# Optimization experiments

Measured on AMD Instinct MI355X. Metric: run time of the kernel, lower is better.

The kernel has to match this reference:

```python
import jax, jax.numpy as jnp
import numpy as np

C = 768
NH = 8
S_SP = 9            # spatial size per axis; seq = 9**3 = 729
HID = (C * 4 * 2) // 3  # 2048, floor(768*8/3)
E = 3               # num_experts
TOPK = 2
EPS = 1e-5


def setup_inputs() -> dict:
    key = jax.random.key(0)
    ks = jax.random.split(key, 10)
    b = 8
    p = lambda k, shape: (jax.random.normal(k, shape, dtype=jnp.float32) * 0.02)
    return {
        "x": jax.random.normal(ks[0], (b, C, S_SP, S_SP, S_SP), dtype=jnp.float32),
        "ln_w": jnp.ones((C, S_SP, S_SP, S_SP), dtype=jnp.float32),
        "ln_b": jnp.zeros((C, S_SP, S_SP, S_SP), dtype=jnp.float32),
        "qkv_w": p(ks[1], (C, 3 * C)),
        "proj_w": p(ks[2], (C, C)),
        "router_w": p(ks[3], (C, E)),
        "gate_w": p(ks[4], (E, C, HID)),
        "up_w": p(ks[5], (E, C, HID)),
        "down_w": p(ks[6], (E, HID, C)),
    }


def _ablock(x, ln_w, ln_b, qkv_w, proj_w, router_w, gate_w, up_w, down_w):
    b, c, t, h, w = x.shape
    s = t * h * w
    dh = c // NH

    # LayerNorm over normalized_shape = (c, t, h, w)
    mean = jnp.mean(x, axis=(1, 2, 3, 4), keepdims=True)
    var = jnp.var(x, axis=(1, 2, 3, 4), keepdims=True)
    y = (x - mean) * jax.lax.rsqrt(var + EPS) * ln_w + ln_b

    # Attention (note: source applies NO 1/sqrt(dh) scaling)
    tok = jnp.transpose(y.reshape(b, c, s), (0, 2, 1))        # (b, s, c)
    qkv = (tok @ qkv_w).reshape(b, s, 3, NH, dh)
    qkv = jnp.transpose(qkv, (2, 0, 3, 1, 4))                  # (3, b, nh, s, dh)
    q, k, v = qkv[0], qkv[1], qkv[2]
    attn = jax.nn.softmax(jnp.einsum("bhsd,bhtd->bhst", q, k), axis=-1)
    o = jnp.einsum("bhst,bhtd->bhsd", attn, v)
    o = jnp.transpose(o, (0, 2, 1, 3)).reshape(b, s, c) @ proj_w  # (b, s, c)
    x = x + jnp.transpose(o, (0, 2, 1)).reshape(b, c, t, h, w)

    # MoE with top-2 routing over SwiGLU experts (dense compute)
    tok = jnp.transpose(x.reshape(b, c, s), (0, 2, 1))         # (b, s, c)
    probs = jax.nn.softmax(tok @ router_w, axis=-1)            # (b, s, E)
    vals, idx = jax.lax.top_k(probs, TOPK)
    vals = vals / jnp.sum(vals, axis=-1, keepdims=True)
    wfull = jnp.sum(jax.nn.one_hot(idx, E, dtype=tok.dtype) * vals[..., None], axis=2)  # (b, s, E)

    g = jnp.einsum("bsc,ech->bseh", tok, gate_w)
    u = jnp.einsum("bsc,ech->bseh", tok, up_w)
    hid = jax.nn.silu(g) * u                                   # (b, s, E, HID)
    eo = jnp.einsum("bseh,ehc->bsec", hid, down_w)             # (b, s, E, c)
    moe_out = jnp.einsum("bsec,bse->bsc", eo, wfull)

    return x + jnp.transpose(moe_out, (0, 2, 1)).reshape(b, c, t, h, w)


def reference(x, ln_w, ln_b, qkv_w, proj_w, router_w, gate_w, up_w, down_w):
    return _ablock(x, ln_w, ln_b, qkv_w, proj_w, router_w, gate_w, up_w, down_w)
```

## Files before the change

kernel.cpp:

```cpp
#include <hip/hip_runtime.h>
#include <hip/hip_bf16.h>

#define C_    768
#define NH_   8
#define DH_   96
#define S_    729
#define B_    8
#define MTOK  5832
#define C3    2304
#define GUN   12288
#define DK    6144
#define SPAD  736
#define NPB   559872

typedef __attribute__((ext_vector_type(8))) short short8;
typedef __attribute__((ext_vector_type(4))) float f32x4;
typedef __attribute__((ext_vector_type(4))) unsigned int uint4v;
typedef __hip_bfloat16 bf16;

__device__ __forceinline__ void gld_lds16(const bf16* g, bf16* l) {
  __builtin_amdgcn_global_load_lds((const __attribute__((address_space(1))) void*)g,
                                   (__attribute__((address_space(3))) void*)l, 16, 0, 0);
}
__device__ __forceinline__ void gld_lds16c(const char* g, char* l) {
  __builtin_amdgcn_global_load_lds((const __attribute__((address_space(1))) void*)g,
                                   (__attribute__((address_space(3))) void*)l, 16, 0, 0);
}

template<int DB>
__device__ __forceinline__ void tile_step(
    char* ldsc, char* ldsw,
    const int rA0, const int rA1, const int rB0, const int rB1,
    const char* pA0, const char* pA1, const char* pA2, const char* pA3,
    const char* pB0, const char* pB1, const char* pB2, const char* pB3,
    const int s1, const int s2, const bool gH1, const bool gH0, const int wmode,
    f32x4 (&acc)[8][4], short8 (&a4)[4][2], short8 (&b4)[4][2])
{
  const int DBO = DB * 65536;
  const int NBO = 65536 - DBO;
  #pragma unroll
  for (int mf = 0; mf < 4; ++mf) {
    a4[mf][0] = *(const short8*)(ldsc + DBO + rA0 + mf*2048);
    a4[mf][1] = *(const short8*)(ldsc + DBO + rA1 + mf*2048);
  }
  #pragma unroll
  for (int nf = 0; nf < 4; ++nf) {
    b4[nf][0] = *(const short8*)(ldsc + DBO + rB0 + nf*2048);
    b4[nf][1] = *(const short8*)(ldsc + DBO + rB1 + nf*2048);
  }
  if (gH1) {
    gld_lds16c(pA2 + s1, ldsw + NBO + 16384);
    gld_lds16c(pA3 + s1, ldsw + NBO + 16384 + 8192);
    gld_lds16c(pB2 + s1, ldsw + NBO + 32768 + 16384);
    gld_lds16c(pB3 + s1, ldsw + NBO + 32768 + 16384 + 8192);
  }
  __builtin_amdgcn_s_setprio(1);
  #pragma unroll
  for (int mf = 0; mf < 4; ++mf)
    #pragma unroll
    for (int nf = 0; nf < 4; ++nf)
      #pragma unroll
      for (int j = 0; j < 2; ++j)
        acc[mf][nf] = __builtin_amdgcn_mfma_f32_16x16x32_bf16(a4[mf][j], b4[nf][j], acc[mf][nf], 0, 0, 0);
  __builtin_amdgcn_s_setprio(0);
  __builtin_amdgcn_s_barrier();
  #pragma unroll
  for (int mi = 0; mi < 4; ++mi) {
    a4[mi][0] = *(const short8*)(ldsc + DBO + rA0 + (4+mi)*2048);
    a4[mi][1] = *(const short8*)(ldsc + DBO + rA1 + (4+mi)*2048);
  }
  __builtin_amdgcn_s_barrier();
  if (gH0) {
    gld_lds16c(pB0 + s2, ldsw + DBO + 32768);
    gld_lds16c(pB1 + s2, ldsw + DBO + 32768 + 8192);
    gld_lds16c(pA0 + s2, ldsw + DBO);
    gld_lds16c(pA1 + s2, ldsw + DBO + 8192);
  }
  __builtin_amdgcn_s_setprio(1);
  #pragma unroll
  for (int mi = 0; mi < 4; ++mi)
    #pragma unroll
    for (int nf = 0; nf < 4; ++nf)
      #pragma unroll
      for (int j = 0; j < 2; ++j)
        acc[4+mi][nf] = __builtin_amdgcn_mfma_f32_16x16x32_bf16(a4[mi][j], b4[nf][j], acc[4+mi][nf], 0, 0, 0);
  __builtin_amdgcn_s_setprio(0);
  if (wmode == 0)      asm volatile("s_waitcnt vmcnt(4)" ::: "memory");
  else if (wmode == 1) asm volatile("s_waitcnt vmcnt(0)" ::: "memory");
  __builtin_amdgcn_s_barrier();
}

__global__ void __launch_bounds__(512, 2)
gemm8(const bf16* __restrict__ A, long a_rs,
      const bf16* __restrict__ Bt, long b_rs,
      float* __restrict__ Cf, bf16* __restrict__ Cb,
      long c_rs, long c_zoff, int M, int N, int Ksub,
      const float* __restrict__ wfull, int mode)
{
  __shared__ __attribute__((aligned(128))) char ldsc[131072];
  const int tid = threadIdx.x;
  const int wid = tid >> 6, lid = tid & 63;
  const int wm = wid >> 2, wn = wid & 3;
  const int fr = lid & 15, g8 = (lid >> 4) * 8;
  const int brow = blockIdx.y * 256, bcol = blockIdx.x * 256;
  const long k0b = (long)blockIdx.z * Ksub * 2;
  const long a_rsb = a_rs * 2, b_rsb = b_rs * 2;
  const int srow = tid >> 3;
  const int scol = ((tid & 7) ^ (srow & 7)) << 4;
  const int NT = Ksub >> 6;
  char* ldsw = ldsc + wid * 1024;

  int ra0_ = brow + srow;        if (ra0_ > M-1) ra0_ = M-1;
  int ra1_ = brow + 64 + srow;   if (ra1_ > M-1) ra1_ = M-1;
  int ra2_ = brow + 128 + srow;  if (ra2_ > M-1) ra2_ = M-1;
  int ra3_ = brow + 192 + srow;  if (ra3_ > M-1) ra3_ = M-1;
  int rb0_ = bcol + srow;        if (rb0_ > N-1) rb0_ = N-1;
  int rb1_ = bcol + 64 + srow;   if (rb1_ > N-1) rb1_ = N-1;
  int rb2_ = bcol + 128 + srow;  if (rb2_ > N-1) rb2_ = N-1;
  int rb3_ = bcol + 192 + srow;  if (rb3_ > N-1) rb3_ = N-1;
  const char* pA0 = (const char*)A + (long)ra0_*a_rsb + k0b + scol;
  const char* pA1 = (const char*)A + (long)ra1_*a_rsb + k0b + scol;
  const char* pA2 = (const char*)A + (long)ra2_*a_rsb + k0b + scol;
  const char* pA3 = (const char*)A + (long)ra3_*a_rsb + k0b + scol;
  const char* pB0 = (const char*)Bt + (long)rb0_*b_rsb + k0b + scol;
  const char* pB1 = (const char*)Bt + (long)rb1_*b_rsb + k0b + scol;
  const char* pB2 = (const char*)Bt + (long)rb2_*b_rsb + k0b + scol;
  const char* pB3 = (const char*)Bt + (long)rb3_*b_rsb + k0b + scol;

  const int swz = (fr & 7) << 4;
  const int cx0 = (g8 * 2) ^ swz;
  const int cx1 = (64 + g8 * 2) ^ swz;
  const int rA0 = (wm*128 + fr)*128 + cx0;
  const int rA1 = (wm*128 + fr)*128 + cx1;
  const int rB0 = 32768 + (wn*64 + fr)*128 + cx0;
  const int rB1 = 32768 + (wn*64 + fr)*128 + cx1;

  f32x4 acc[8][4] = {};
  short8 a4[4][2], b4[4][2];

  gld_lds16c(pA0, ldsw);
  gld_lds16c(pA1, ldsw + 8192);
  gld_lds16c(pA2, ldsw + 16384);
  gld_lds16c(pA3, ldsw + 16384 + 8192);
  gld_lds16c(pB0, ldsw + 32768);
  gld_lds16c(pB1, ldsw + 32768 + 8192);
  gld_lds16c(pB2, ldsw + 32768 + 16384);
  gld_lds16c(pB3, ldsw + 32768 + 16384 + 8192);
  gld_lds16c(pA0 + 128, ldsw + 65536);
  gld_lds16c(pA1 + 128, ldsw + 65536 + 8192);
  gld_lds16c(pB0 + 128, ldsw + 65536 + 32768);
  gld_lds16c(pB1 + 128, ldsw + 65536 + 32768 + 8192);
  asm volatile("s_waitcnt vmcnt(4)" ::: "memory");
  __builtin_amdgcn_s_barrier();

  for (int tp = 0; tp < NT; tp += 2) {
    const bool g2 = (tp + 2) < NT;
    tile_step<0>(ldsc, ldsw, rA0, rA1, rB0, rB1,
                 pA0, pA1, pA2, pA3, pB0, pB1, pB2, pB3,
                 128, 256, true, g2, g2 ? 0 : 1, acc, a4, b4);
    tile_step<1>(ldsc, ldsw, rA0, rA1, rB0, rB1,
                 pA0, pA1, pA2, pA3, pB0, pB1, pB2, pB3,
                 256, 384, g2, g2, g2 ? 0 : 2, acc, a4, b4);
    if (g2) {
      pA0 += 256; pA1 += 256; pA2 += 256; pA3 += 256;
      pB0 += 256; pB1 += 256; pB2 += 256; pB3 += 256;
    }
  }

  const int rg = (lid >> 4) * 4;
  if (mode == 3) {
    #pragma unroll
    for (int mf = 0; mf < 8; ++mf) {
      #pragma unroll
      for (int np = 0; np < 2; ++np) {
        const int hb = (bcol + wn*64 + np*32) >> 5;
        const int h = hb*16 + fr;
        const int e = h >> 11;
        #pragma unroll
        for (int j = 0; j < 4; ++j) {
          const int row = brow + wm*128 + mf*16 + rg + j;
          if (row < M) {
            float g = acc[mf][2*np][j];
            float u = acc[mf][2*np+1][j];
            float w = wfull[row*3 + e];
            float sg = g / (1.f + __expf(-g));
            Cb[(long)row*c_rs + h] = __float2bfloat16(sg * u * w);
          }
        }
      }
    }
  } else {
    #pragma unroll
    for (int mf = 0; mf < 8; ++mf) {
      #pragma unroll
      for (int nf = 0; nf < 4; ++nf) {
        const int col = bcol + wn*64 + nf*16 + fr;
        if (col < N) {
          #pragma unroll
          for (int j = 0; j < 4; ++j) {
            const int row = brow + wm*128 + mf*16 + rg + j;
            if (row < M) {
              long off = (long)blockIdx.z*c_zoff + (long)row*c_rs + col;
              if (mode == 0) Cb[off] = __float2bfloat16(acc[mf][nf][j]);
              else           Cf[off] = acc[mf][nf][j];
            }
          }
        }
      }
    }
  }
}

__global__ void __launch_bounds__(256)
gemm3_bt(const bf16* __restrict__ Ah, const bf16* __restrict__ Al,
         long a_rs, long a_oo, long a_oi,
         const bf16* __restrict__ Bth, const bf16* __restrict__ Btl,
         long b_rs, long b_oo, long b_oi,
         float* __restrict__ Cf, bf16* __restrict__ Ch, bf16* __restrict__ Cl,
         long c_rs, long c_oo, long c_oi,
         int M, int N, int K, int nlim, int zdiv)
{
  __shared__ bf16 lAh[4096];
  __shared__ bf16 lAl[4096];
  __shared__ bf16 lBh[4096];
  __shared__ bf16 lBl[4096];
  const int tid = threadIdx.x;
  const int wid = tid >> 6;
  const int lid = tid & 63;
  const int z = blockIdx.z;
  const int zo = z / zdiv, zi = z - zo*zdiv;
  const long aoff = (long)zo*a_oo + (long)zi*a_oi;
  const long boff = (long)zo*b_oo + (long)zi*b_oi;
  const long cbase = (long)zo*c_oo + (long)zi*c_oi;
  const int brow = blockIdx.y * 128;
  const int bcol = blockIdx.x * 128;

  const int ch0 = tid, ch1 = tid + 256;
  int ra0 = brow + (ch0 >> 2); if (ra0 > M-1) ra0 = M-1;
  int ra1 = brow + (ch1 >> 2); if (ra1 > M-1) ra1 = M-1;
  int rb0 = bcol + (ch0 >> 2); if (rb0 > N-1) rb0 = N-1;
  int rb1 = bcol + (ch1 >> 2); if (rb1 > N-1) rb1 = N-1;
  const int sw = ((ch0 ^ (ch0 >> 2)) & 3) * 8;
  const long ia0 = aoff + (long)ra0*a_rs + sw;
  const long ia1 = aoff + (long)ra1*a_rs + sw;
  const long ib0 = boff + (long)rb0*b_rs + sw;
  const long ib1 = boff + (long)rb1*b_rs + sw;
  bf16* dAh0 = (bf16*)((char*)lAh + wid*1024);
  bf16* dAh1 = (bf16*)((char*)lAh + 4096 + wid*1024);
  bf16* dAl0 = (bf16*)((char*)lAl + wid*1024);
  bf16* dAl1 = (bf16*)((char*)lAl + 4096 + wid*1024);
  bf16* dBh0 = (bf16*)((char*)lBh + wid*1024);
  bf16* dBh1 = (bf16*)((char*)lBh + 4096 + wid*1024);
  bf16* dBl0 = (bf16*)((char*)lBl + wid*1024);
  bf16* dBl1 = (bf16*)((char*)lBl + 4096 + wid*1024);

  f32x4 acc[4][4] = {};
  const int wm = wid >> 1, wn = wid & 1;
  const int fr = lid & 15, g8 = (lid >> 4) * 8;
  const int gx = g8 ^ ((lid & 3) << 3);

  for (int kt = 0; kt < K; kt += 32) {
    __syncthreads();
    gld_lds16(Ah + ia0 + kt, dAh0);
    gld_lds16(Ah + ia1 + kt, dAh1);
    gld_lds16(Al + ia0 + kt, dAl0);
    gld_lds16(Al + ia1 + kt, dAl1);
    gld_lds16(Bth + ib0 + kt, dBh0);
    gld_lds16(Bth + ib1 + kt, dBh1);
    gld_lds16(Btl + ib0 + kt, dBl0);
    gld_lds16(Btl + ib1 + kt, dBl1);
    __syncthreads();
    short8 fah[4], fal[4], fbh[4], fbl[4];
    #pragma unroll
    for (int m = 0; m < 4; ++m) {
      int ro = (wm*64 + m*16 + fr)*32 + gx;
      fah[m] = *(const short8*)&lAh[ro];
      fal[m] = *(const short8*)&lAl[ro];
    }
    #pragma unroll
    for (int n = 0; n < 4; ++n) {
      int ro = (wn*64 + n*16 + fr)*32 + gx;
      fbh[n] = *(const short8*)&lBh[ro];
      fbl[n] = *(const short8*)&lBl[ro];
    }
    #pragma unroll
    for (int m = 0; m < 4; ++m)
      #pragma unroll
      for (int n = 0; n < 4; ++n) {
        acc[m][n] = __builtin_amdgcn_mfma_f32_16x16x32_bf16(fal[m], fbh[n], acc[m][n], 0, 0, 0);
        acc[m][n] = __builtin_amdgcn_mfma_f32_16x16x32_bf16(fah[m], fbl[n], acc[m][n], 0, 0, 0);
        acc[m][n] = __builtin_amdgcn_mfma_f32_16x16x32_bf16(fah[m], fbh[n], acc[m][n], 0, 0, 0);
      }
  }

  const int rg = (lid >> 4) * 4;
  #pragma unroll
  for (int m = 0; m < 4; ++m) {
    #pragma unroll
    for (int n = 0; n < 4; ++n) {
      const int col = bcol + wn*64 + n*16 + fr;
      if (col < nlim) {
        #pragma unroll
        for (int j = 0; j < 4; ++j) {
          const int row = brow + wm*64 + m*16 + rg + j;
          if (row < M) {
            long off = cbase + (long)row*c_rs + col;
            float v = acc[m][n][j];
            if (Cl) {
              bf16 h = __float2bfloat16(v);
              Ch[off] = h;
              Cl[off] = __float2bfloat16(v - __bfloat162float(h));
            } else if (Ch) {
              Ch[off] = __float2bfloat16(v);
            } else {
              Cf[off] = v;
            }
          }
        }
      }
    }
  }
}

__global__ void wtrans(const float* __restrict__ in, bf16* __restrict__ out,
                       int R, int Cc, long in_rs, long out_rs, long in_bs, long out_bs,
                       int ilv, int radd)
{
  __shared__ float tile[32][33];
  in  += (long)blockIdx.z * in_bs;
  out += (long)blockIdx.z * out_bs;
  int r0 = blockIdx.y*32, c0 = blockIdx.x*32;
  int tx = threadIdx.x, ty = threadIdx.y;
  #pragma unroll
  for (int i = 0; i < 32; i += 8) {
    int r = r0 + ty + i, c = c0 + tx;
    if (r < R && c < Cc) tile[ty+i][tx] = in[(long)r*in_rs + c];
  }
  __syncthreads();
  #pragma unroll
  for (int i = 0; i < 32; i += 8) {
    int ro = c0 + ty + i, co = r0 + tx;
    if (ro < Cc && co < R) {
      int rr = ilv ? (((ro >> 4) << 5) + (ro & 15) + radd) : ro;
      out[(long)rr*out_rs + co] = __float2bfloat16(tile[tx][ty+i]);
    }
  }
}

__global__ void wtrans3(const float* __restrict__ in, bf16* __restrict__ oh, bf16* __restrict__ ol,
                        int R, int Cc, long in_rs, long out_rs)
{
  __shared__ float tile[32][33];
  int r0 = blockIdx.y*32, c0 = blockIdx.x*32;
  int tx = threadIdx.x, ty = threadIdx.y;
  #pragma unroll
  for (int i = 0; i < 32; i += 8) {
    int r = r0 + ty + i, c = c0 + tx;
    if (r < R && c < Cc) tile[ty+i][tx] = in[(long)r*in_rs + c];
  }
  __syncthreads();
  #pragma unroll
  for (int i = 0; i < 32; i += 8) {
    int ro = c0 + ty + i, co = r0 + tx;
    if (ro < Cc && co < R) {
      float v = tile[tx][ty+i];
      bf16 h = __float2bfloat16(v);
      long o = (long)ro*out_rs + co;
      oh[o] = h;
      ol[o] = __float2bfloat16(v - __bfloat162float(h));
    }
  }
}

__global__ void ln_partial(const float* __restrict__ x, float* __restrict__ part) {
  int b = blockIdx.y, blk = blockIdx.x;
  const float* xb = x + (long)b*NPB;
  int start = blk * 4374;
  float s = 0.f, ss = 0.f;
  for (int i = start + threadIdx.x; i < start + 4374; i += 256) {
    float v = xb[i]; s += v; ss += v*v;
  }
  #pragma unroll
  for (int o = 32; o; o >>= 1) { s += __shfl_down(s, o); ss += __shfl_down(ss, o); }
  __shared__ float red[2][4];
  int wid = threadIdx.x >> 6, lid = threadIdx.x & 63;
  if (lid == 0) { red[0][wid] = s; red[1][wid] = ss; }
  __syncthreads();
  if (threadIdx.x == 0) {
    float S = 0.f, SS = 0.f;
    for (int w = 0; w < 4; ++w) { S += red[0][w]; SS += red[1][w]; }
    part[(b*128 + blk)*2] = S; part[(b*128 + blk)*2 + 1] = SS;
  }
}

__global__ void ln_final(const float* __restrict__ part, float* __restrict__ stats) {
  int b = blockIdx.x, lid = threadIdx.x;
  float s = 0.f, ss = 0.f;
  for (int i = lid; i < 128; i += 64) { s += part[(b*128+i)*2]; ss += part[(b*128+i)*2+1]; }
  #pragma unroll
  for (int o = 32; o; o >>= 1) { s += __shfl_down(s, o); ss += __shfl_down(ss, o); }
  if (lid == 0) {
    float mean = s / (float)NPB;
    float var = ss / (float)NPB - mean*mean;
    stats[b*2] = mean; stats[b*2+1] = rsqrtf(var + 1e-5f);
  }
}

__global__ void ln_apply3(const float* __restrict__ x, const float* __restrict__ lnw,
                          const float* __restrict__ lnb, const float* __restrict__ stats,
                          bf16* __restrict__ th, bf16* __restrict__ tl, long ts)
{
  __shared__ float tile[32][33];
  int b = blockIdx.z;
  int s0 = blockIdx.x*32, c0 = blockIdx.y*32;
  float mean = stats[b*2], rstd = stats[b*2+1];
  int tx = threadIdx.x, ty = threadIdx.y;
  #pragma unroll
  for (int i = 0; i < 32; i += 8) {
    int c = c0 + ty + i, s = s0 + tx;
    if (s < S_) {
      long o = (long)c*S_ + s;
      tile[ty+i][tx] = (x[(long)b*NPB + o] - mean)*rstd*lnw[o] + lnb[o];
    }
  }
  __syncthreads();
  #pragma unroll
  for (int i = 0; i < 32; i += 8) {
    int s = s0 + ty + i, c = c0 + tx;
    if (s < S_) {
      float v = tile[tx][ty+i];
      bf16 h = __float2bfloat16(v);
      long o = ((long)b*S_ + s)*ts + c;
      th[o] = h;
      tl[o] = __float2bfloat16(v - __bfloat162float(h));
    }
  }
}

__global__ void vtrans2(const bf16* __restrict__ qkvh, const bf16* __restrict__ qkvl,
                        bf16* __restrict__ VTh, bf16* __restrict__ VTl)
{
  __shared__ float tile[32][33];
  int z = blockIdx.z;
  const bf16* qkv = (z < 64) ? qkvh : qkvl;
  bf16* VT = (z < 64) ? VTh : VTl;
  int zz = z & 63;
  int bb = zz >> 3, h = zz & 7;
  const bf16* v = qkv + (long)bb*S_*C3 + 1536 + h*DH_;
  bf16* o = VT + (long)zz*DH_*SPAD;
  int t0 = blockIdx.y*32, d0 = blockIdx.x*32;
  int tx = threadIdx.x, ty = threadIdx.y;
  #pragma unroll
  for (int i = 0; i < 32; i += 8) {
    int t = t0 + ty + i, d = d0 + tx;
    float val = 0.f;
    if (t < S_ && d < DH_) val = __bfloat162float(v[(long)t*C3 + d]);
    tile[ty+i][tx] = val;
  }
  __syncthreads();
  #pragma unroll
  for (int i = 0; i < 32; i += 8) {
    int d = d0 + ty + i, t = t0 + tx;
    if (d < DH_ && t < SPAD) o[(long)d*SPAD + t] = __float2bfloat16(tile[tx][ty+i]);
  }
}

__global__ void softmax3p(bf16* __restrict__ scores, int nrows) {
  int row = blockIdx.x*4 + (threadIdx.x >> 6);
  if (row >= nrows) return;
  int lid = threadIdx.x & 63;
  bf16* ph = scores + (long)row*2*SPAD;
  bf16* pl = ph + SPAD;
  float vals[12];
  float mx = -1e30f;
  #pragma unroll
  for (int i = 0; i < 12; ++i) {
    int t = i*64 + lid;
    float v = -1e30f;
    if (t < S_) v = __bfloat162float(ph[t]) + __bfloat162float(pl[t]);
    vals[i] = v; mx = fmaxf(mx, v);
  }
  #pragma unroll
  for (int o = 32; o; o >>= 1) mx = fmaxf(mx, __shfl_xor(mx, o));
  float sum = 0.f;
  #pragma unroll
  for (int i = 0; i < 12; ++i) { float e = __expf(vals[i] - mx); vals[i] = e; sum += e; }
  #pragma unroll
  for (int o = 32; o; o >>= 1) sum += __shfl_xor(sum, o);
  float inv = 1.f / sum;
  #pragma unroll
  for (int i = 0; i < 12; ++i) {
    int t = i*64 + lid;
    if (t < SPAD) {
      float p = (t < S_) ? vals[i]*inv : 0.f;
      bf16 h = __float2bfloat16(p);
      ph[t] = h;
      pl[t] = __float2bfloat16(p - __bfloat162float(h));
    }
  }
}

__global__ void tadd1(const float* __restrict__ x, const float* __restrict__ oproj,
                      float* __restrict__ xattn, bf16* __restrict__ tok2,
                      float* __restrict__ tok2f)
{
  __shared__ float t_o[32][33];
  __shared__ float t_x[32][33];
  int b = blockIdx.z;
  int s0 = blockIdx.x*32, c0 = blockIdx.y*32;
  int tx = threadIdx.x, ty = threadIdx.y;
  #pragma unroll
  for (int i = 0; i < 32; i += 8) {
    int s = s0 + ty + i;
    if (s < S_) t_o[ty+i][tx] = oproj[((long)b*S_ + s)*C_ + c0 + tx];
    int s2 = s0 + tx;
    if (s2 < S_) t_x[ty+i][tx] = x[(long)b*NPB + (long)(c0+ty+i)*S_ + s2];
  }
  __syncthreads();
  #pragma unroll
  for (int i = 0; i < 32; i += 8) {
    int s = s0 + tx, c = c0 + ty + i;
    if (s < S_) xattn[(long)b*NPB + (long)c*S_ + s] = t_x[ty+i][tx] + t_o[tx][ty+i];
    int s2 = s0 + ty + i, c2 = c0 + tx;
    if (s2 < S_) {
      float v = t_x[tx][ty+i] + t_o[ty+i][tx];
      long o = ((long)b*S_ + s2)*C_ + c2;
      tok2[o] = __float2bfloat16(v);
      tok2f[o] = v;
    }
  }
}

__global__ void tadd2(const float* __restrict__ xattn, const bf16* __restrict__ prt,
                      float* __restrict__ out)
{
  __shared__ float t_m[32][33];
  __shared__ float t_x[32][33];
  int b = blockIdx.z;
  int s0 = blockIdx.x*32, c0 = blockIdx.y*32;
  int tx = threadIdx.x, ty = threadIdx.y;
  #pragma unroll
  for (int i = 0; i < 32; i += 8) {
    int s = s0 + ty + i;
    if (s < S_) {
      const bf16* p = prt + ((long)b*S_ + s)*768 + c0 + tx;
      float acc = 0.f;
      #pragma unroll
      for (int z = 0; z < 8; ++z) acc += __bfloat162float(p[(long)z*MTOK*768]);
      t_m[ty+i][tx] = acc;
    }
    int s2 = s0 + tx;
    if (s2 < S_) t_x[ty+i][tx] = xattn[(long)b*NPB + (long)(c0+ty+i)*S_ + s2];
  }
  __syncthreads();
  #pragma unroll
  for (int i = 0; i < 32; i += 8) {
    int s = s0 + tx, c = c0 + ty + i;
    if (s < S_) out[(long)b*NPB + (long)c*S_ + s] = t_x[ty+i][tx] + t_m[tx][ty+i];
  }
}

__global__ void router_k(const float* __restrict__ tok2f, const float* __restrict__ rw,
                         float* __restrict__ wfull)
{
  int t = blockIdx.x*4 + (threadIdx.x >> 6);
  if (t >= MTOK) return;
  int lid = threadIdx.x & 63;
  const float* tk = tok2f + (long)t*C_;
  float a0 = 0.f, a1 = 0.f, a2 = 0.f;
  for (int i = lid; i < C_; i += 64) {
    float v = tk[i];
    a0 += v*rw[i*3+0]; a1 += v*rw[i*3+1]; a2 += v*rw[i*3+2];
  }
  #pragma unroll
  for (int o = 32; o; o >>= 1) {
    a0 += __shfl_xor(a0, o); a1 += __shfl_xor(a1, o); a2 += __shfl_xor(a2, o);
  }
  if (lid == 0) {
    float m = fmaxf(a0, fmaxf(a1, a2));
    float e0 = __expf(a0-m), e1 = __expf(a1-m), e2 = __expf(a2-m);
    int emin = 0; float pm = e0;
    if (e1 <= pm) { pm = e1; emin = 1; }
    if (e2 <= pm) { pm = e2; emin = 2; }
    float rest = e0 + e1 + e2 - pm;
    wfull[t*3+0] = (emin == 0) ? 0.f : e0/rest;
    wfull[t*3+1] = (emin == 1) ? 0.f : e1/rest;
    wfull[t*3+2] = (emin == 2) ? 0.f : e2/rest;
  }
}

static inline void launch_gemm3(hipStream_t st,
    const bf16* Ah, const bf16* Al, long a_rs, long a_oo, long a_oi,
    const bf16* Bh, const bf16* Bl, long b_rs, long b_oo, long b_oi,
    float* Cf, bf16* Ch, bf16* Cl, long c_rs, long c_oo, long c_oi,
    int M, int N, int K, int nlim, int zdiv, int nz)
{
  dim3 g((N + 127)/128, (M + 127)/128, nz);
  gemm3_bt<<<g, 256, 0, st>>>(Ah, Al, a_rs, a_oo, a_oi, Bh, Bl, b_rs, b_oo, b_oi,
                              Cf, Ch, Cl, c_rs, c_oo, c_oi, M, N, K, nlim, zdiv);
}

extern "C" void kernel_launch(void* const* d_in, const int* in_sizes, int n_in,
                              void* d_out, int out_size, void* d_ws, size_t ws_size,
                              hipStream_t stream)
{
  const float* x      = (const float*)d_in[0];
  const float* ln_w   = (const float*)d_in[1];
  const float* ln_b   = (const float*)d_in[2];
  const float* qkv_w  = (const float*)d_in[3];
  const float* proj_w = (const float*)d_in[4];
  const float* rout_w = (const float*)d_in[5];
  const float* gate_w = (const float*)d_in[6];
  const float* up_w   = (const float*)d_in[7];
  const float* down_w = (const float*)d_in[8];
  float* out = (float*)d_out;

  char* ws = (char*)d_ws;
  size_t off = 0;
  auto alloc = [&](size_t bytes) { size_t r = off; off += (bytes + 255) & ~(size_t)255; return r; };

  size_t o_stats = alloc(8*2*4);
  size_t o_part  = alloc(8*128*2*4);
  size_t o_wfull = alloc((size_t)MTOK*3*4);
  size_t o_qkvTh = alloc((size_t)C3*C_*2);
  size_t o_qkvTl = alloc((size_t)C3*C_*2);
  size_t o_prjTh = alloc((size_t)C_*C_*2);
  size_t o_prjTl = alloc((size_t)C_*C_*2);
  size_t o_guT   = alloc((size_t)GUN*C_*2);
  size_t o_downT = alloc((size_t)C_*DK*2);
  size_t o_xattn = alloc((size_t)B_*NPB*4);
  size_t o_tok2  = alloc((size_t)MTOK*C_*2);
  size_t o_tok2f = alloc((size_t)MTOK*C_*4);
  size_t big0 = off;
  size_t o_qkvh  = alloc((size_t)MTOK*C3*2);
  size_t o_qkvl  = alloc((size_t)MTOK*C3*2);
  size_t o_VTh   = alloc((size_t)64*DH_*SPAD*2);
  size_t o_VTl   = alloc((size_t)64*DH_*SPAD*2);
  size_t o_aoh   = alloc((size_t)MTOK*C_*2);
  size_t o_aol   = alloc((size_t)MTOK*C_*2);
  size_t o_union = alloc((size_t)32*S_*SPAD*4);
  size_t endA = off;
  off = big0;
  size_t o_hid = alloc((size_t)MTOK*DK*2);
  size_t o_prt = alloc((size_t)8*MTOK*768*2);
  size_t endB = off;
  size_t needed = endA > endB ? endA : endB;
  if (ws_size < needed) return;

  float* stats  = (float*)(ws + o_stats);
  float* part   = (float*)(ws + o_part);
  float* wfull  = (float*)(ws + o_wfull);
  bf16*  qkvTh  = (bf16*)(ws + o_qkvTh);
  bf16*  qkvTl  = (bf16*)(ws + o_qkvTl);
  bf16*  prjTh  = (bf16*)(ws + o_prjTh);
  bf16*  prjTl  = (bf16*)(ws + o_prjTl);
  bf16*  guT    = (bf16*)(ws + o_guT);
  bf16*  downT  = (bf16*)(ws + o_downT);
  float* xattn  = (float*)(ws + o_xattn);
  bf16*  tok2   = (bf16*)(ws + o_tok2);
  float* tok2f  = (float*)(ws + o_tok2f);
  bf16*  qkvh   = (bf16*)(ws + o_qkvh);
  bf16*  qkvl   = (bf16*)(ws + o_qkvl);
  bf16*  VTh    = (bf16*)(ws + o_VTh);
  bf16*  VTl    = (bf16*)(ws + o_VTl);
  bf16*  aoh    = (bf16*)(ws + o_aoh);
  bf16*  aol    = (bf16*)(ws + o_aol);
  bf16*  tokh   = (bf16*)(ws + o_union);
  bf16*  tokl   = (bf16*)(ws + o_union + (size_t)MTOK*C_*2);
  bf16*  Pbase  = (bf16*)(ws + o_union);
  float* oproj  = (float*)(ws + o_union);
  bf16*  hidden = (bf16*)(ws + o_hid);
  bf16*  prt    = (bf16*)(ws + o_prt);

  dim3 b32(32, 8);

  wtrans3<<<dim3(72,24,1), b32, 0, stream>>>(qkv_w,  qkvTh, qkvTl, 768, 2304, 2304, 768);
  wtrans3<<<dim3(24,24,1), b32, 0, stream>>>(proj_w, prjTh, prjTl, 768, 768,  768,  768);
  wtrans<<<dim3(64,24,3), b32, 0, stream>>>(gate_w, guT, 768, 2048, 2048, 768,
                                            (long)768*2048, (long)4096*768, 1, 0);
  wtrans<<<dim3(64,24,3), b32, 0, stream>>>(up_w, guT, 768, 2048, 2048, 768,
                                            (long)768*2048, (long)4096*768, 1, 16);
  wtrans<<<dim3(24,64,3), b32, 0, stream>>>(down_w, downT, 2048, 768, 768, 6144,
                                            (long)2048*768, 2048, 0, 0);

  ln_partial<<<dim3(128,8), 256, 0, stream>>>(x, part);
  ln_final<<<8, 64, 0, stream>>>(part, stats);
  ln_apply3<<<dim3(23,24,8), b32, 0, stream>>>(x, ln_w, ln_b, stats, tokh, tokl, C_);

  launch_gemm3(stream, tokh, tokl, C_, 0, 0, qkvTh, qkvTl, C_, 0, 0,
               nullptr, qkvh, qkvl, C3, 0, 0, MTOK, C3, C_, C3, 1, 1);

  vtrans2<<<dim3(3,23,128), b32, 0, stream>>>(qkvh, qkvl, VTh, VTl);

  for (int c = 0; c < 2; ++c) {
    const long qoff = (long)(4*c)*S_*C3;
    launch_gemm3(stream,
        qkvh + qoff, qkvl + qoff, C3, (long)S_*C3, DH_,
        qkvh + qoff + 768, qkvl + qoff + 768, C3, (long)S_*C3, DH_,
        nullptr, Pbase, Pbase + SPAD, 2*SPAD, (long)8*S_*2*SPAD, (long)S_*2*SPAD,
        S_, S_, DH_, SPAD, 8, 32);
    softmax3p<<<5832, 256, 0, stream>>>(Pbase, 32*S_);
    launch_gemm3(stream,
        Pbase, Pbase + SPAD, 2*SPAD, (long)8*S_*2*SPAD, (long)S_*2*SPAD,
        VTh + (size_t)c*32*DH_*SPAD, VTl + (size_t)c*32*DH_*SPAD, SPAD,
        (long)8*DH_*SPAD, (long)DH_*SPAD,
        nullptr, aoh + (size_t)(4*c)*S_*C_, aol + (size_t)(4*c)*S_*C_,
        C_, (long)S_*C_, DH_,
        S_, DH_, SPAD, DH_, 8, 32);
  }

  launch_gemm3(stream, aoh, aol, C_, 0, 0, prjTh, prjTl, C_, 0, 0,
               oproj, nullptr, nullptr, C_, 0, 0, MTOK, C_, C_, C_, 1, 1);

  tadd1<<<dim3(23,24,8), b32, 0, stream>>>(x, oproj, xattn, tok2, tok2f);

  router_k<<<1458, 256, 0, stream>>>(tok2f, rout_w, wfull);

  gemm8<<<dim3(GUN/256, 23, 1), 512, 0, stream>>>(
      tok2, C_, guT, C_, nullptr, hidden, DK, 0, MTOK, GUN, C_, wfull, 3);

  gemm8<<<dim3(C_/256, 23, 8), 512, 0, stream>>>(
      hidden, DK, downT, DK, nullptr, prt, 768, (long)MTOK*768, MTOK, C_, DK/8,
      nullptr, 0);

  tadd2<<<dim3(23,24,8), b32, 0, stream>>>(xattn, prt, out);
}
```

Measured before the change: 782.5 us.

## Replace 256x256 MoE GEMM with smaller 128x128 tile, double-buffered kernel

Swaps the 512-thread 256x256-tile GEMM used for the MoE gate/up and down projections for a 256-thread 128x128-tile kernel. The new kernel uses a 32-wide K step, 32KB of LDS with a simpler double buffer, and a full vmcnt(0) wait on every step. The aim is more blocks and higher occupancy (3 blocks per CU) and less tail waste on the 5832-row M dimension. In exchange, each block reuses less data from global memory, loads happen in smaller chunks, and the finer-grained pipeline synchronises more often.

Result: faster. 745.9 us (-4.7%).

```diff
diff --git a/kernel.cpp b/kernel.cpp
--- a/kernel.cpp
+++ b/kernel.cpp
@@ -27,150 +27,90 @@
                                    (__attribute__((address_space(3))) void*)l, 16, 0, 0);
 }
 
-template<int DB>
-__device__ __forceinline__ void tile_step(
-    char* ldsc, char* ldsw,
-    const int rA0, const int rA1, const int rB0, const int rB1,
-    const char* pA0, const char* pA1, const char* pA2, const char* pA3,
-    const char* pB0, const char* pB1, const char* pB2, const char* pB3,
-    const int s1, const int s2, const bool gH1, const bool gH0, const int wmode,
-    f32x4 (&acc)[8][4], short8 (&a4)[4][2], short8 (&b4)[4][2])
-{
-  const int DBO = DB * 65536;
-  const int NBO = 65536 - DBO;
-  #pragma unroll
-  for (int mf = 0; mf < 4; ++mf) {
-    a4[mf][0] = *(const short8*)(ldsc + DBO + rA0 + mf*2048);
-    a4[mf][1] = *(const short8*)(ldsc + DBO + rA1 + mf*2048);
-  }
-  #pragma unroll
-  for (int nf = 0; nf < 4; ++nf) {
-    b4[nf][0] = *(const short8*)(ldsc + DBO + rB0 + nf*2048);
-    b4[nf][1] = *(const short8*)(ldsc + DBO + rB1 + nf*2048);
-  }
-  if (gH1) {
-    gld_lds16c(pA2 + s1, ldsw + NBO + 16384);
-    gld_lds16c(pA3 + s1, ldsw + NBO + 16384 + 8192);
-    gld_lds16c(pB2 + s1, ldsw + NBO + 32768 + 16384);
-    gld_lds16c(pB3 + s1, ldsw + NBO + 32768 + 16384 + 8192);
-  }
+template<int DBO>
+__device__ __forceinline__ void g97_step(
+    char* ldsc, char* ldsw, const int rA, const int rB, const int cx,
+    const char*& pA0, const char*& pA1, const char*& pB0, const char*& pB1,
+    const bool stage, f32x4 (&acc)[4][4])
+{
+  const int NBO = 16384 - DBO;
+  if (stage) {
+    gld_lds16c(pA0, ldsw + NBO);
+    gld_lds16c(pA1, ldsw + NBO + 4096);
+    gld_lds16c(pB0, ldsw + NBO + 8192);
+    gld_lds16c(pB1, ldsw + NBO + 12288);
+    pA0 += 64; pA1 += 64; pB0 += 64; pB1 += 64;
+  }
+  short8 a4[4], b4[4];
+  #pragma unroll
+  for (int mf = 0; mf < 4; ++mf)
+    a4[mf] = *(const short8*)(ldsc + DBO + rA + mf*1024 + cx);
+  #pragma unroll
+  for (int nf = 0; nf < 4; ++nf)
+    b4[nf] = *(const short8*)(ldsc + DBO + rB + nf*1024 + cx);
   __builtin_amdgcn_s_setprio(1);
   #pragma unroll
   for (int mf = 0; mf < 4; ++mf)
     #pragma unroll
     for (int nf = 0; nf < 4; ++nf)
-      #pragma unroll
-      for (int j = 0; j < 2; ++j)
-        acc[mf][nf] = __builtin_amdgcn_mfma_f32_16x16x32_bf16(a4[mf][j], b4[nf][j], acc[mf][nf], 0, 0, 0);
+      acc[mf][nf] = __builtin_amdgcn_mfma_f32_16x16x32_bf16(a4[mf], b4[nf], acc[mf][nf], 0, 0, 0);
   __builtin_amdgcn_s_setprio(0);
+  asm volatile("s_waitcnt vmcnt(0)" ::: "memory");
   __builtin_amdgcn_s_barrier();
-  #pragma unroll
-  for (int mi = 0; mi < 4; ++mi) {
-    a4[mi][0] = *(const short8*)(ldsc + DBO + rA0 + (4+mi)*2048);
-    a4[mi][1] = *(const short8*)(ldsc + DBO + rA1 + (4+mi)*2048);
-  }
-  __builtin_amdgcn_s_barrier();
-  if (gH0) {
-    gld_lds16c(pB0 + s2, ldsw + DBO + 32768);
-    gld_lds16c(pB1 + s2, ldsw + DBO + 32768 + 8192);
-    gld_lds16c(pA0 + s2, ldsw + DBO);
-    gld_lds16c(pA1 + s2, ldsw + DBO + 8192);
-  }
-  __builtin_amdgcn_s_setprio(1);
-  #pragma unroll
-  for (int mi = 0; mi < 4; ++mi)
-    #pragma unroll
-    for (int nf = 0; nf < 4; ++nf)
-      #pragma unroll
-      for (int j = 0; j < 2; ++j)
-        acc[4+mi][nf] = __builtin_amdgcn_mfma_f32_16x16x32_bf16(a4[mi][j], b4[nf][j], acc[4+mi][nf], 0, 0, 0);
-  __builtin_amdgcn_s_setprio(0);
-  if (wmode == 0)      asm volatile("s_waitcnt vmcnt(4)" ::: "memory");
-  else if (wmode == 1) asm volatile("s_waitcnt vmcnt(0)" ::: "memory");
-  __builtin_amdgcn_s_barrier();
-}
-
-__global__ void __launch_bounds__(512, 2)
-gemm8(const bf16* __restrict__ A, long a_rs,
-      const bf16* __restrict__ Bt, long b_rs,
-      float* __restrict__ Cf, bf16* __restrict__ Cb,
-      long c_rs, long c_zoff, int M, int N, int Ksub,
-      const float* __restrict__ wfull, int mode)
-{
-  __shared__ __attribute__((aligned(128))) char ldsc[131072];
+}
+
+__global__ void __launch_bounds__(256, 3)
+gemm97(const bf16* __restrict__ A, long a_rs,
+       const bf16* __restrict__ Bt, long b_rs,
+       float* __restrict__ Cf, bf16* __restrict__ Cb,
+       long c_rs, long c_zoff, int M, int N, int Ksub,
+       const float* __restrict__ wfull, int mode)
+{
+  __shared__ __attribute__((aligned(128))) char ldsc[32768];
   const int tid = threadIdx.x;
   const int wid = tid >> 6, lid = tid & 63;
-  const int wm = wid >> 2, wn = wid & 3;
+  const int wm = wid >> 1, wn = wid & 1;
   const int fr = lid & 15, g8 = (lid >> 4) * 8;
-  const int brow = blockIdx.y * 256, bcol = blockIdx.x * 256;
+  const int brow = blockIdx.y * 128, bcol = blockIdx.x * 128;
   const long k0b = (long)blockIdx.z * Ksub * 2;
   const long a_rsb = a_rs * 2, b_rsb = b_rs * 2;
-  const int srow = tid >> 3;
-  const int scol = ((tid & 7) ^ (srow & 7)) << 4;
-  const int NT = Ksub >> 6;
+  const int srow = tid >> 2;
+  const int scol = ((tid & 3) ^ (srow & 3)) << 4;
+  const int NT = Ksub >> 5;
   char* ldsw = ldsc + wid * 1024;
 
-  int ra0_ = brow + srow;        if (ra0_ > M-1) ra0_ = M-1;
-  int ra1_ = brow + 64 + srow;   if (ra1_ > M-1) ra1_ = M-1;
-  int ra2_ = brow + 128 + srow;  if (ra2_ > M-1) ra2_ = M-1;
-  int ra3_ = brow + 192 + srow;  if (ra3_ > M-1) ra3_ = M-1;
-  int rb0_ = bcol + srow;        if (rb0_ > N-1) rb0_ = N-1;
-  int rb1_ = bcol + 64 + srow;   if (rb1_ > N-1) rb1_ = N-1;
-  int rb2_ = bcol + 128 + srow;  if (rb2_ > N-1) rb2_ = N-1;
-  int rb3_ = bcol + 192 + srow;  if (rb3_ > N-1) rb3_ = N-1;
+  int ra0_ = brow + srow;       if (ra0_ > M-1) ra0_ = M-1;
+  int ra1_ = brow + 64 + srow;  if (ra1_ > M-1) ra1_ = M-1;
+  int rb0_ = bcol + srow;       if (rb0_ > N-1) rb0_ = N-1;
+  int rb1_ = bcol + 64 + srow;  if (rb1_ > N-1) rb1_ = N-1;
   const char* pA0 = (const char*)A + (long)ra0_*a_rsb + k0b + scol;
   const char* pA1 = (const char*)A + (long)ra1_*a_rsb + k0b + scol;
-  const char* pA2 = (const char*)A + (long)ra2_*a_rsb + k0b + scol;
-  const char* pA3 = (const char*)A + (long)ra3_*a_rsb + k0b + scol;
   const char* pB0 = (const char*)Bt + (long)rb0_*b_rsb + k0b + scol;
   const char* pB1 = (const char*)Bt + (long)rb1_*b_rsb + k0b + scol;
-  const char* pB2 = (const char*)Bt + (long)rb2_*b_rsb + k0b + scol;
-  const char* pB3 = (const char*)Bt + (long)rb3_*b_rsb + k0b + scol;
-
-  const int swz = (fr & 7) << 4;
-  const int cx0 = (g8 * 2) ^ swz;
-  const int cx1 = (64 + g8 * 2) ^ swz;
-  const int rA0 = (wm*128 + fr)*128 + cx0;
-  const int rA1 = (wm*128 + fr)*128 + cx1;
-  const int rB0 = 32768 + (wn*64 + fr)*128 + cx0;
-  const int rB1 = 32768 + (wn*64 + fr)*128 + cx1;
-
-  f32x4 acc[8][4] = {};
-  short8 a4[4][2], b4[4][2];
+
+  const int cx = (g8*2) ^ ((fr & 3) << 4);
+  const int rA = (wm*64 + fr)*64;
+  const int rB = 8192 + (wn*64 + fr)*64;
+
+  f32x4 acc[4][4] = {};
 
   gld_lds16c(pA0, ldsw);
-  gld_lds16c(pA1, ldsw + 8192);
-  gld_lds16c(pA2, ldsw + 16384);
-  gld_lds16c(pA3, ldsw + 16384 + 8192);
-  gld_lds16c(pB0, ldsw + 32768);
-  gld_lds16c(pB1, ldsw + 32768 + 8192);
-  gld_lds16c(pB2, ldsw + 32768 + 16384);
-  gld_lds16c(pB3, ldsw + 32768 + 16384 + 8192);
-  gld_lds16c(pA0 + 128, ldsw + 65536);
-  gld_lds16c(pA1 + 128, ldsw + 65536 + 8192);
-  gld_lds16c(pB0 + 128, ldsw + 65536 + 32768);
-  gld_lds16c(pB1 + 128, ldsw + 65536 + 32768 + 8192);
-  asm volatile("s_waitcnt vmcnt(4)" ::: "memory");
+  gld_lds16c(pA1, ldsw + 4096);
+  gld_lds16c(pB0, ldsw + 8192);
+  gld_lds16c(pB1, ldsw + 12288);
+  pA0 += 64; pA1 += 64; pB0 += 64; pB1 += 64;
+  asm volatile("s_waitcnt vmcnt(0)" ::: "memory");
   __builtin_amdgcn_s_barrier();
 
   for (int tp = 0; tp < NT; tp += 2) {
-    const bool g2 = (tp + 2) < NT;
-    tile_step<0>(ldsc, ldsw, rA0, rA1, rB0, rB1,
-                 pA0, pA1, pA2, pA3, pB0, pB1, pB2, pB3,
-                 128, 256, true, g2, g2 ? 0 : 1, acc, a4, b4);
-    tile_step<1>(ldsc, ldsw, rA0, rA1, rB0, rB1,
-                 pA0, pA1, pA2, pA3, pB0, pB1, pB2, pB3,
-                 256, 384, g2, g2, g2 ? 0 : 2, acc, a4, b4);
-    if (g2) {
-      pA0 += 256; pA1 += 256; pA2 += 256; pA3 += 256;
-      pB0 += 256; pB1 += 256; pB2 += 256; pB3 += 256;
-    }
+    g97_step<0>(ldsc, ldsw, rA, rB, cx, pA0, pA1, pB0, pB1, true, acc);
+    g97_step<16384>(ldsc, ldsw, rA, rB, cx, pA0, pA1, pB0, pB1, (tp + 2) < NT, acc);
   }
 
   const int rg = (lid >> 4) * 4;
   if (mode == 3) {
     #pragma unroll
-    for (int mf = 0; mf < 8; ++mf) {
+    for (int mf = 0; mf < 4; ++mf) {
       #pragma unroll
       for (int np = 0; np < 2; ++np) {
         const int hb = (bcol + wn*64 + np*32) >> 5;
@@ -178,7 +118,7 @@
         const int e = h >> 11;
         #pragma unroll
         for (int j = 0; j < 4; ++j) {
-          const int row = brow + wm*128 + mf*16 + rg + j;
+          const int row = brow + wm*64 + mf*16 + rg + j;
           if (row < M) {
             float g = acc[mf][2*np][j];
             float u = acc[mf][2*np+1][j];
@@ -191,14 +131,14 @@
     }
   } else {
     #pragma unroll
-    for (int mf = 0; mf < 8; ++mf) {
+    for (int mf = 0; mf < 4; ++mf) {
       #pragma unroll
       for (int nf = 0; nf < 4; ++nf) {
         const int col = bcol + wn*64 + nf*16 + fr;
         if (col < N) {
           #pragma unroll
           for (int j = 0; j < 4; ++j) {
-            const int row = brow + wm*128 + mf*16 + rg + j;
+            const int row = brow + wm*64 + mf*16 + rg + j;
             if (row < M) {
               long off = (long)blockIdx.z*c_zoff + (long)row*c_rs + col;
               if (mode == 0) Cb[off] = __float2bfloat16(acc[mf][nf][j]);
@@ -716,10 +656,10 @@
 
   router_k<<<1458, 256, 0, stream>>>(tok2f, rout_w, wfull);
 
-  gemm8<<<dim3(GUN/256, 23, 1), 512, 0, stream>>>(
+  gemm97<<<dim3(GUN/128, 46, 1), 256, 0, stream>>>(
       tok2, C_, guT, C_, nullptr, hidden, DK, 0, MTOK, GUN, C_, wfull, 3);
 
-  gemm8<<<dim3(C_/256, 23, 8), 512, 0, stream>>>(
+  gemm97<<<dim3(C_/128, 46, 8), 256, 0, stream>>>(
       hidden, DK, downT, DK, nullptr, prt, 768, (long)MTOK*768, MTOK, C_, DK/8,
       nullptr, 0);
 
```
